# Optimization experiments

Hardware: AMD Instinct MI355X
Metric: run time of the kernel (lower is better)

## Reference

```python
import jax, jax.numpy as jnp
import numpy as np

N = 4096          # neurons (and input size)
T = 300           # timesteps = time / dt
DT = 1.0
TIME = 300.0
REST = 0.0
RESET = 0.0
THRESH = 10.0
REFRAC = 1.0
TC_DECAY = 100.0


def setup_inputs() -> dict:
    key = jax.random.key(0)
    k1, k2, k3 = jax.random.split(key, 3)
    inp = jax.random.randint(k1, (T, N), 0, 2).astype(jnp.int32)   # binary spike train
    w = jax.random.normal(k2, (N, N), jnp.float32) * 0.05
    w_rec = jax.random.normal(k3, (N, N), jnp.float32) * 0.05
    return {"inp": inp, "w": w, "w_rec": w_rec}


def _simulate(inp, w, w_rec):
    # Faithful port of LIFLayer.__call__ applied over T timesteps via lax.scan.
    # Per step (original order): x = inp@w + s_prev@w_rec; v = decay*(v-rest)+rest;
    # x[rt>0]=0; rt-=dt; v+=x; s=(v>=thresh); t[s]=ts*dt/time; rt[s]=refrac; v[s]=reset.
    decay = jnp.exp(jnp.float32(-DT / TC_DECAY))
    n = w.shape[1]
    v0 = jnp.full((n,), RESET, jnp.float32)
    rt0 = jnp.zeros((n,), jnp.float32)
    s0 = jnp.zeros((n,), jnp.float32)   # previous-step spikes (s[:, -1])
    t0 = jnp.ones((n,), jnp.float32)    # t initialized to ones (store_all_spikes=False)

    def step(carry, xs):
        v, rt, s_prev, t_prev = carry
        inp_t, ts = xs
        x = inp_t.astype(jnp.float32) @ w + s_prev @ w_rec   # [n]
        v = decay * (v - REST) + REST                        # v_ext = 0 (default)
        x = jnp.where(rt > 0, jnp.float32(0.0), x)           # refractory gating
        rt = rt - DT
        v = v + x
        spike = v >= THRESH
        s = spike.astype(jnp.float32)
        t_new = jnp.where(spike, ts.astype(jnp.float32) * DT / TIME, t_prev)
        rt = jnp.where(spike, jnp.float32(REFRAC), rt)
        v = jnp.where(spike, jnp.float32(RESET), v)
        return (v, rt, s, t_new), (s, t_new, v)

    _, (s_all, t_all, v_all) = jax.lax.scan(
        step, (v0, rt0, s0, t0), (inp, jnp.arange(inp.shape[0]))
    )
    return s_all, t_all, v_all


def reference(inp, w, w_rec):
    # Returns per-timestep spikes [T,n], spike-time record [T,n], and membrane
    # potential trace [T,n] (post-reset v, the internal state the kernel computes).
    return _simulate(inp, w, w_rec)
```

## Files before the change

### kernel.cpp

```cpp
#include <hip/hip_runtime.h>
#include <hip/hip_cooperative_groups.h>

namespace cg = cooperative_groups;

#define NN    4096
#define TT    300
#define TPAD  320
#define TCH   20
#define GRID  256
#define BLOCK 1024
#define NREP  16
#define DECAYF 0.9900498337491681f
#define THRESHF 10.0f

#define WS_REQ ((size_t)NN*TPAD*4*2 + (size_t)NREP*2*256*4)

__device__ __forceinline__ uint4 llc_load_v4(const uint4* p) {
    uint4 r;
    asm volatile("global_load_dwordx4 %0, %1, off sc0 sc1\n\t"
                 "s_waitcnt vmcnt(0)"
                 : "=v"(r) : "v"(p) : "memory");
    return r;
}

__global__ __launch_bounds__(BLOCK, 4)
void lif_sim(const int* __restrict__ inp, const float* __restrict__ w,
             const float* __restrict__ w_rec, float* __restrict__ out,
             float* __restrict__ ws)
{
    float* inpT = ws;
    float* X    = ws + (size_t)NN * TPAD;
    unsigned int* maskrep = (unsigned int*)(X + (size_t)TPAD * NN);

    float* s_all = out;
    float* t_all = out + (size_t)TT * NN;
    float* v_all = out + (size_t)2 * TT * NN;

    cg::grid_group grid = cg::this_grid();
    const int tid  = threadIdx.x;
    const int bid  = blockIdx.x;
    const int gtid = bid * BLOCK + tid;

    __shared__ __align__(16) float smem[10240];
    unsigned int* mask_sh = (unsigned int*)smem;
    float*        red_sh  = smem + 256;

    if (gtid < NREP * 2 * 256) maskrep[gtid] = 0u;
    if (gtid < NN * 32) {
        int j = gtid >> 5, tl = gtid & 31;
        if (tl < TPAD - TT) inpT[(size_t)j * TPAD + TT + tl] = 0.0f;
    }
    for (int idx = gtid; idx < TT * NN; idx += GRID * BLOCK) {
        int t = idx >> 12, j = idx & (NN - 1);
        inpT[(size_t)j * TPAD + t] = (float)inp[idx];
    }
    grid.sync();

    {
        const int ct  = bid >> 4;
        const int cc  = bid & 15;
        const int c1  = tid & 255;
        const int jp  = tid >> 8;
        const int col = cc * 256 + c1;
        const int t0  = ct * TCH;
        const int j0  = jp * 1024;
        const float* wp = w + col;
        float acc[20];
#pragma unroll
        for (int k = 0; k < 20; ++k) acc[k] = 0.0f;
        for (int j = j0; j < j0 + 1024; ++j) {
            float wj = wp[(size_t)j * NN];
            const float* iprow = inpT + (size_t)j * TPAD + t0;
#pragma unroll
            for (int k = 0; k < 20; ++k) acc[k] = fmaf(iprow[k], wj, acc[k]);
        }
#pragma unroll
        for (int half = 0; half < 2; ++half) {
#pragma unroll
            for (int k = 0; k < 10; ++k) smem[(jp * 10 + k) * 256 + c1] = acc[half * 10 + k];
            __syncthreads();
            if (jp == 0) {
#pragma unroll
                for (int k = 0; k < 10; ++k) {
                    float s = smem[k * 256 + c1] + smem[(10 + k) * 256 + c1]
                            + smem[(20 + k) * 256 + c1] + smem[(30 + k) * 256 + c1];
                    X[(size_t)(t0 + half * 10 + k) * NN + col] = s;
                }
            }
            __syncthreads();
        }
    }
    grid.sync();

    const int lane = tid & 63;
    const int wave = tid >> 6;
    const int c    = tid & 15;
    const int r    = tid >> 4;
    const int col  = bid * 16 + c;

    float v = 0.0f, tv = 1.0f;
    int sprev = 0;
    const float* wrc = w_rec + col + (size_t)(r << 6) * NN;
    unsigned int* myrep = maskrep + ((bid & 15) * 2) * 256;

    float xreg = 0.0f;
    if (tid < 16) xreg = X[col];

    for (int t = 0; t < TT; ++t) {
        if (wave == 0) {
            const uint4* pp = (const uint4*)(myrep + (t & 1) * 256) + lane;
            const unsigned int ut = (unsigned int)t;
            uint4 q;
            for (;;) {
                q = llc_load_v4(pp);
                unsigned int bad = ((q.x >> 16) ^ ut) | ((q.y >> 16) ^ ut)
                                 | ((q.z >> 16) ^ ut) | ((q.w >> 16) ^ ut);
                if (__all(bad == 0u)) break;
            }
            ((uint4*)mask_sh)[lane] = q;
        }
        __syncthreads();

        unsigned long long M;
        {
            const unsigned int* ms = mask_sh + (r << 2);
            M = ((unsigned long long)(ms[0] & 0xFFFFu))
              | ((unsigned long long)(ms[1] & 0xFFFFu) << 16)
              | ((unsigned long long)(ms[2] & 0xFFFFu) << 32)
              | ((unsigned long long)(ms[3] & 0xFFFFu) << 48);
        }
        float acc0 = 0.0f, acc1 = 0.0f, acc2 = 0.0f, acc3 = 0.0f;
        while (M) {
            float l0, l1 = 0.0f, l2 = 0.0f, l3 = 0.0f,
                  l4 = 0.0f, l5 = 0.0f, l6 = 0.0f, l7 = 0.0f;
            int b0 = __builtin_ctzll(M); M &= M - 1;
            l0 = wrc[(size_t)b0 * NN];
            if (M) { int b = __builtin_ctzll(M); M &= M - 1; l1 = wrc[(size_t)b * NN]; }
            if (M) { int b = __builtin_ctzll(M); M &= M - 1; l2 = wrc[(size_t)b * NN]; }
            if (M) { int b = __builtin_ctzll(M); M &= M - 1; l3 = wrc[(size_t)b * NN]; }
            if (M) { int b = __builtin_ctzll(M); M &= M - 1; l4 = wrc[(size_t)b * NN]; }
            if (M) { int b = __builtin_ctzll(M); M &= M - 1; l5 = wrc[(size_t)b * NN]; }
            if (M) { int b = __builtin_ctzll(M); M &= M - 1; l6 = wrc[(size_t)b * NN]; }
            if (M) { int b = __builtin_ctzll(M); M &= M - 1; l7 = wrc[(size_t)b * NN]; }
            acc0 += l0 + l4; acc1 += l1 + l5; acc2 += l2 + l6; acc3 += l3 + l7;
        }
        float part = (acc0 + acc1) + (acc2 + acc3);
        part += __shfl_xor(part, 16, 64);
        part += __shfl_xor(part, 32, 64);
        if (lane < 16) red_sh[wave * 17 + lane] = part;
        __syncthreads();

        if (wave == 0) {
            const int cw = lane & 15, h = lane >> 4;
            const float* sp = red_sh + h * 4 * 17 + cw;
            float s = (sp[0] + sp[17]) + (sp[34] + sp[51]);
            s += __shfl_xor(s, 16, 64);
            s += __shfl_xor(s, 32, 64);

            bool spike = false;
            if (lane < 16) {
                float x = xreg + s;
                v *= DECAYF;
                if (sprev) x = 0.0f;
                v += x;
                spike = v >= THRESHF;
                if (spike) { tv = (float)t * (1.0f / 300.0f); v = 0.0f; }
                sprev = spike ? 1 : 0;
            }
            unsigned long long bal = __ballot(spike);
            if (lane == 0) {
                unsigned int word = ((unsigned int)(t + 1) << 16)
                                  | (unsigned int)(bal & 0xFFFFull);
                const int par = (t + 1) & 1;
#pragma unroll
                for (int rep = 0; rep < NREP; ++rep)
                    __hip_atomic_store(maskrep + (rep * 2 + par) * 256 + bid, word,
                                       __ATOMIC_RELAXED, __HIP_MEMORY_SCOPE_AGENT);
            }
            if (lane < 16) {
                size_t o = (size_t)t * NN + col;
                s_all[o] = spike ? 1.0f : 0.0f;
                t_all[o] = tv;
                v_all[o] = v;
                if (t + 1 < TT) xreg = X[(size_t)(t + 1) * NN + col];
            }
        }
    }
}

extern "C" void kernel_launch(void* const* d_in, const int* in_sizes, int n_in,
                              void* d_out, int out_size, void* d_ws, size_t ws_size,
                              hipStream_t stream) {
    if (ws_size < WS_REQ) return;
    const int*   inp   = (const int*)d_in[0];
    const float* w     = (const float*)d_in[1];
    const float* w_rec = (const float*)d_in[2];
    float* out = (float*)d_out;
    float* ws  = (float*)d_ws;
    void* args[] = {(void*)&inp, (void*)&w, (void*)&w_rec, (void*)&out, (void*)&ws};
    hipLaunchCooperativeKernel((const void*)lif_sim, dim3(GRID), dim3(BLOCK),
                               args, 0, stream);
}
```

Before: 1.640 ms.

## Cache half of each block's recurrent weight columns in LDS

At the start of the recurrent phase, each block copies rows 0-2047 of its 16 w_rec columns into dynamic shared memory, using a padded stride. Threads covering those rows gather spiking-neuron weights from LDS, while the remaining rows still gather from global memory with a deeper 16-way unroll. Blocks are also remapped to column groups with an interleaved mapping, which changes which columns land together on each die, and the spike-mask slot index now follows that mapping. The aim is to halve the scattered global loads on the per-timestep critical path. In exchange it needs about 150KB of dynamic LDS per block and a one-time copy, and it leaves the LDS half and the global half of each block with uneven work.

Result: no change. 1.621 ms (-1.2%).

```diff
diff --git a/kernel.cpp b/kernel.cpp
--- a/kernel.cpp
+++ b/kernel.cpp
@@ -10,8 +10,13 @@
 #define GRID  256
 #define BLOCK 1024
 #define NREP  16
+#define WSTRIDE 18
+#define HROWS 2048
 #define DECAYF 0.9900498337491681f
 #define THRESHF 10.0f
+
+#define WLDS_BYTES (HROWS * WSTRIDE * 4)
+#define DSM_BYTES  (WLDS_BYTES + 1024 + 16 * 17 * 4)
 
 #define WS_REQ ((size_t)NN*TPAD*4*2 + (size_t)NREP*2*256*4)
 
@@ -41,9 +46,11 @@
     const int bid  = blockIdx.x;
     const int gtid = bid * BLOCK + tid;
 
-    __shared__ __align__(16) float smem[10240];
-    unsigned int* mask_sh = (unsigned int*)smem;
-    float*        red_sh  = smem + 256;
+    extern __shared__ __align__(16) unsigned char dsm[];
+    float*        smem    = (float*)dsm;
+    float*        wlds    = (float*)dsm;
+    unsigned int* mask_sh = (unsigned int*)(dsm + WLDS_BYTES);
+    float*        red_sh  = (float*)(dsm + WLDS_BYTES + 1024);
 
     if (gtid < NREP * 2 * 256) maskrep[gtid] = 0u;
     if (gtid < NN * 32) {
@@ -92,15 +99,32 @@
     }
     grid.sync();
 
+    const int colgrp = ((bid & 7) << 5) | (bid >> 3);
+    const int col0   = colgrp * 16;
     const int lane = tid & 63;
     const int wave = tid >> 6;
     const int c    = tid & 15;
     const int r    = tid >> 4;
-    const int col  = bid * 16 + c;
+    const int col  = col0 + c;
+
+    {
+        const int srow = tid >> 2;
+        const int c4   = (tid & 3) << 2;
+#pragma unroll
+        for (int pass = 0; pass < 8; ++pass) {
+            const int row = pass * 256 + srow;
+            const float4 q = *(const float4*)(w_rec + (size_t)row * NN + col0 + c4);
+            float2* dst = (float2*)(wlds + row * WSTRIDE + c4);
+            dst[0] = make_float2(q.x, q.y);
+            dst[1] = make_float2(q.z, q.w);
+        }
+    }
+    __syncthreads();
 
     float v = 0.0f, tv = 1.0f;
     int sprev = 0;
     const float* wrc = w_rec + col + (size_t)(r << 6) * NN;
+    const int ldsbase = (r << 6) * WSTRIDE + c;
     unsigned int* myrep = maskrep + ((bid & 15) * 2) * 256;
 
     float xreg = 0.0f;
@@ -130,19 +154,42 @@
               | ((unsigned long long)(ms[3] & 0xFFFFu) << 48);
         }
         float acc0 = 0.0f, acc1 = 0.0f, acc2 = 0.0f, acc3 = 0.0f;
-        while (M) {
-            float l0, l1 = 0.0f, l2 = 0.0f, l3 = 0.0f,
-                  l4 = 0.0f, l5 = 0.0f, l6 = 0.0f, l7 = 0.0f;
-            int b0 = __builtin_ctzll(M); M &= M - 1;
-            l0 = wrc[(size_t)b0 * NN];
-            if (M) { int b = __builtin_ctzll(M); M &= M - 1; l1 = wrc[(size_t)b * NN]; }
-            if (M) { int b = __builtin_ctzll(M); M &= M - 1; l2 = wrc[(size_t)b * NN]; }
-            if (M) { int b = __builtin_ctzll(M); M &= M - 1; l3 = wrc[(size_t)b * NN]; }
-            if (M) { int b = __builtin_ctzll(M); M &= M - 1; l4 = wrc[(size_t)b * NN]; }
-            if (M) { int b = __builtin_ctzll(M); M &= M - 1; l5 = wrc[(size_t)b * NN]; }
-            if (M) { int b = __builtin_ctzll(M); M &= M - 1; l6 = wrc[(size_t)b * NN]; }
-            if (M) { int b = __builtin_ctzll(M); M &= M - 1; l7 = wrc[(size_t)b * NN]; }
-            acc0 += l0 + l4; acc1 += l1 + l5; acc2 += l2 + l6; acc3 += l3 + l7;
+        if (r < 32) {
+            while (M) {
+                float l0, l1 = 0.0f, l2 = 0.0f, l3 = 0.0f;
+                int b0 = __builtin_ctzll(M); M &= M - 1;
+                l0 = wlds[ldsbase + b0 * WSTRIDE];
+                if (M) { int b = __builtin_ctzll(M); M &= M - 1; l1 = wlds[ldsbase + b * WSTRIDE]; }
+                if (M) { int b = __builtin_ctzll(M); M &= M - 1; l2 = wlds[ldsbase + b * WSTRIDE]; }
+                if (M) { int b = __builtin_ctzll(M); M &= M - 1; l3 = wlds[ldsbase + b * WSTRIDE]; }
+                acc0 += l0 + l2; acc1 += l1 + l3;
+            }
+        } else {
+            while (M) {
+                float l0,        l1 = 0.0f, l2 = 0.0f, l3 = 0.0f,
+                      l4 = 0.0f, l5 = 0.0f, l6 = 0.0f, l7 = 0.0f,
+                      l8 = 0.0f, l9 = 0.0f, l10 = 0.0f, l11 = 0.0f,
+                      l12 = 0.0f, l13 = 0.0f, l14 = 0.0f, l15 = 0.0f;
+                int b0 = __builtin_ctzll(M); M &= M - 1;
+                l0 = wrc[(size_t)b0 * NN];
+                if (M) { int b = __builtin_ctzll(M); M &= M - 1; l1  = wrc[(size_t)b * NN]; }
+                if (M) { int b = __builtin_ctzll(M); M &= M - 1; l2  = wrc[(size_t)b * NN]; }
+                if (M) { int b = __builtin_ctzll(M); M &= M - 1; l3  = wrc[(size_t)b * NN]; }
+                if (M) { int b = __builtin_ctzll(M); M &= M - 1; l4  = wrc[(size_t)b * NN]; }
+                if (M) { int b = __builtin_ctzll(M); M &= M - 1; l5  = wrc[(size_t)b * NN]; }
+                if (M) { int b = __builtin_ctzll(M); M &= M - 1; l6  = wrc[(size_t)b * NN]; }
+                if (M) { int b = __builtin_ctzll(M); M &= M - 1; l7  = wrc[(size_t)b * NN]; }
+                if (M) { int b = __builtin_ctzll(M); M &= M - 1; l8  = wrc[(size_t)b * NN]; }
+                if (M) { int b = __builtin_ctzll(M); M &= M - 1; l9  = wrc[(size_t)b * NN]; }
+                if (M) { int b = __builtin_ctzll(M); M &= M - 1; l10 = wrc[(size_t)b * NN]; }
+                if (M) { int b = __builtin_ctzll(M); M &= M - 1; l11 = wrc[(size_t)b * NN]; }
+                if (M) { int b = __builtin_ctzll(M); M &= M - 1; l12 = wrc[(size_t)b * NN]; }
+                if (M) { int b = __builtin_ctzll(M); M &= M - 1; l13 = wrc[(size_t)b * NN]; }
+                if (M) { int b = __builtin_ctzll(M); M &= M - 1; l14 = wrc[(size_t)b * NN]; }
+                if (M) { int b = __builtin_ctzll(M); M &= M - 1; l15 = wrc[(size_t)b * NN]; }
+                acc0 += l0 + l4;  acc1 += l1 + l5;  acc2 += l2 + l6;  acc3 += l3 + l7;
+                acc0 += l8 + l12; acc1 += l9 + l13; acc2 += l10 + l14; acc3 += l11 + l15;
+            }
         }
         float part = (acc0 + acc1) + (acc2 + acc3);
         part += __shfl_xor(part, 16, 64);
@@ -174,7 +221,7 @@
                 const int par = (t + 1) & 1;
 #pragma unroll
                 for (int rep = 0; rep < NREP; ++rep)
-                    __hip_atomic_store(maskrep + (rep * 2 + par) * 256 + bid, word,
+                    __hip_atomic_store(maskrep + (rep * 2 + par) * 256 + colgrp, word,
                                        __ATOMIC_RELAXED, __HIP_MEMORY_SCOPE_AGENT);
             }
             if (lane < 16) {
@@ -197,7 +244,9 @@
     const float* w_rec = (const float*)d_in[2];
     float* out = (float*)d_out;
     float* ws  = (float*)d_ws;
+    hipFuncSetAttribute((const void*)lif_sim,
+                        hipFuncAttributeMaxDynamicSharedMemorySize, DSM_BYTES);
     void* args[] = {(void*)&inp, (void*)&w, (void*)&w_rec, (void*)&out, (void*)&ws};
     hipLaunchCooperativeKernel((const void*)lif_sim, dim3(GRID), dim3(BLOCK),
-                               args, 0, stream);
+                               args, DSM_BYTES, stream);
 }
```
